# Optimization experiments

Measured on AMD Instinct MI355X. Metric: run time of the kernel, lower is better.

The kernel has to match this reference:

```python
import jax, jax.numpy as jnp
import numpy as np

BN_EPS = 1e-5


def _binary_activation(x):
    # forward value = sign(x); gradient flows through piecewise poly o3 (STE)
    s = jnp.sign(x)
    o1 = jnp.where(x < -1.0, -1.0, x * x + 2.0 * x)
    o2 = jnp.where(x < 0.0, o1, -x * x + 2.0 * x)
    o3 = jnp.where(x < 1.0, o2, 1.0)
    return jax.lax.stop_gradient(s - o3) + o3


def _binarize_weights(w):
    # sign_function: fwd 2*(w>0)-1, bwd identity (STE)
    sgn = 2.0 * (w > 0.0).astype(w.dtype) - 1.0
    wb = jax.lax.stop_gradient(sgn - w) + w
    # detached per-output-channel scale: mean |w| over (in, kh, kw)
    scale = jax.lax.stop_gradient(jnp.mean(jnp.abs(w), axis=(1, 2, 3), keepdims=True))
    return scale * wb


def setup_inputs() -> dict:
    key = jax.random.key(0)
    k1, k2, k3 = jax.random.split(key, 3)
    C = 64
    x = jax.random.normal(k1, (32, C, 112, 112), dtype=jnp.float32)
    w = jax.random.uniform(k2, (C, C, 3, 3), dtype=jnp.float32) * 0.001
    return {
        "x": x,
        "b0": jnp.zeros((1, C, 1, 1), jnp.float32),
        "w": w,
        "gamma": jnp.ones((C,), jnp.float32),
        "beta": jnp.zeros((C,), jnp.float32),
        "b1": jnp.zeros((1, C, 1, 1), jnp.float32),
        "alpha": jnp.full((C,), 0.25, jnp.float32),  # PReLU default init
        "b2": jnp.zeros((1, C, 1, 1), jnp.float32),
    }


def reference(x, b0, w, gamma, beta, b1, alpha, b2):
    residual = x
    out = x + b0                       # move0
    out = _binary_activation(out)      # binary activation
    bw = _binarize_weights(w)
    out = jax.lax.conv_general_dilated(
        out, bw, window_strides=(1, 1), padding=[(1, 1), (1, 1)],
        dimension_numbers=("NCHW", "OIHW", "NCHW"))
    # BatchNorm2d in training mode (batch stats, biased variance)
    mu = jnp.mean(out, axis=(0, 2, 3), keepdims=True)
    var = jnp.var(out, axis=(0, 2, 3), keepdims=True)
    g = gamma.reshape(1, -1, 1, 1)
    b = beta.reshape(1, -1, 1, 1)
    out = (out - mu) * jax.lax.rsqrt(var + BN_EPS) * g + b
    out = out + residual
    out = out + b1                     # move1
    a = alpha.reshape(1, -1, 1, 1)
    out = jnp.where(out > 0, out, a * out)  # PReLU
    out = out + b2                     # move2
    return out
```

## Files before the change

### kernel.cpp

```cpp
#include <hip/hip_runtime.h>
#include <stdint.h>

#define C 64
#define HH 112
#define WWD 112
#define HW (HH*WWD)
#define NB 32
#define MTOT (NB*HW)
#define PPR 56
#define PPI 6272
#define PACK_BLKS 1568
#define CONV_BLKS 25
#define OH 32
#define FL4 3136

typedef unsigned long long u64t;

__global__ __launch_bounds__(256) void k_prep_pack(
        const float* __restrict__ x, const float* __restrict__ b0,
        const float* __restrict__ w,
        uint64_t* __restrict__ xp,
        uint64_t* __restrict__ wbits, float* __restrict__ wscale,
        int* __restrict__ corrP, int* __restrict__ ps, u64t* __restrict__ pq) {
    int bid = blockIdx.x;
    if (bid < PACK_BLKS) {
        int n = bid / 49;
        int pix = (bid % 49) * 256 + threadIdx.x;
        uint64_t p = 0;
        const float* xb = x + (size_t)n * C * HW + pix;
        #pragma unroll
        for (int c = 0; c < C; ++c) {
            float v = xb[(size_t)c * HW] + b0[c];
            p |= (uint64_t)(v > 0.f) << c;
        }
        xp[(size_t)n*HW + pix] = p;
    } else {
        int tid = threadIdx.x;
        int o = bid - PACK_BLKS;
        if (tid < 64) {
            int i = tid;
            const float* wp = w + ((size_t)o*C + i)*9;
            float s = 0.f;
            uint64_t b[9];
            #pragma unroll
            for (int k = 0; k < 9; ++k) {
                float v = wp[k];
                s += fabsf(v);
                b[k] = __ballot(v > 0.f);
            }
            #pragma unroll
            for (int off = 32; off > 0; off >>= 1) s += __shfl_down(s, off);
            if (i == 0) {
                wscale[o] = s * (1.0f/576.0f);
                int pq9[9];
                #pragma unroll
                for (int k = 0; k < 9; ++k) {
                    wbits[o*9+k] = b[k];
                    pq9[k] = __popcll(b[k]);
                }
                for (int rc = 0; rc < 3; ++rc)
                    for (int cc = 0; cc < 3; ++cc) {
                        int corr = 0;
                        for (int kr = 0; kr < 3; ++kr)
                            for (int kc = 0; kc < 3; ++kc) {
                                bool oob = (rc==0 && kr==0) || (rc==2 && kr==2) ||
                                           (cc==0 && kc==0) || (cc==2 && kc==2);
                                if (oob) corr += 64 - 2*pq9[kr*3+kc];
                            }
                        corrP[(rc*3+cc)*C + o] = 576 - corr;
                    }
            }
        } else if (bid == PACK_BLKS) {
            for (int i = tid - 64; i < C*8; i += 192) { ps[i] = 0; pq[i] = 0ull; }
        }
    }
}

__global__ __launch_bounds__(256) void k_convstats(
        const uint64_t* __restrict__ xp, const uint64_t* __restrict__ wbits,
        const int* __restrict__ corrP, int* __restrict__ ps, u64t* __restrict__ pq,
        uint32_t* __restrict__ cv) {
    __shared__ uint64_t sq[OH*9];
    __shared__ int scor[9*OH];
    __shared__ int lsw[4][OH];
    __shared__ int lqw[4][OH];
    const int obase = blockIdx.z * OH;
    for (int i = threadIdx.x; i < OH*9; i += 256) sq[i] = wbits[obase*9 + i];
    for (int i = threadIdx.x; i < 9*OH; i += 256) {
        int r = i / OH, oo = i - r*OH;
        scor[i] = corrP[r*C + obase + oo];
    }
    __syncthreads();

    int n = blockIdx.y;
    int pr = blockIdx.x * 256 + threadIdx.x;
    int act = pr < PPI;
    int prc = act ? pr : (PPI - 1);
    int row = prc / PPR;
    int j   = prc - row * PPR;
    int c0  = 2 * j;
    const uint64_t* base = xp + (size_t)n * HW;
    uint64_t P[12];
    #pragma unroll
    for (int r = 0; r < 3; ++r) {
        int rr = row + r - 1;
        bool okr = (rr >= 0) & (rr < HH);
        #pragma unroll
        for (int c = 0; c < 4; ++c) {
            int cc = c0 + c - 1;
            bool ok = okr & (cc >= 0) & (cc < WWD);
            P[r*4+c] = ok ? base[(size_t)rr * WWD + cc] : 0ull;
        }
    }
    int rc   = (row == 0) ? 0 : ((row == HH-1) ? 2 : 1);
    int reg0 = (rc*3 + ((c0 == 0) ? 0 : 1)) * OH;
    int reg1 = (rc*3 + ((c0 == WWD-2) ? 2 : 1)) * OH;
    int wid = threadIdx.x >> 6, lane = threadIdx.x & 63;

    uint32_t* op = cv + ((size_t)n * C + obase) * HW + prc;

    #pragma unroll 2
    for (int oo = 0; oo < OH; ++oo) {
        const uint64_t* q = &sq[oo*9];
        int a0 = 0, a1 = 0;
        #pragma unroll
        for (int r = 0; r < 3; ++r) {
            #pragma unroll
            for (int c = 0; c < 3; ++c) {
                uint64_t qk = q[r*3+c];
                a0 += __popcll(P[r*4+c]   ^ qk);
                a1 += __popcll(P[r*4+c+1] ^ qk);
            }
        }
        int v0 = scor[reg0 + oo] - 2*a0;
        int v1 = scor[reg1 + oo] - 2*a1;
        if (act) op[(size_t)oo * HW] =
            (uint32_t)(uint16_t)v0 | ((uint32_t)(uint16_t)v1 << 16);
        int s  = act ? (v0 + v1) : 0;
        int qq = act ? (v0*v0 + v1*v1) : 0;
        #pragma unroll
        for (int off = 1; off < 64; off <<= 1) {
            s  += __shfl_xor(s,  off);
            qq += __shfl_xor(qq, off);
        }
        if (lane == 0) { lsw[wid][oo] = s; lqw[wid][oo] = qq; }
    }
    __syncthreads();
    int t = threadIdx.x;
    int bkt = blockIdx.y & 7;
    if (t < OH) {
        int st = lsw[0][t] + lsw[1][t] + lsw[2][t] + lsw[3][t];
        atomicAdd(&ps[(obase + t)*8 + bkt], st);
    } else if (t < 2*OH) {
        int oo = t - OH;
        unsigned int qt = (unsigned)lqw[0][oo] + (unsigned)lqw[1][oo]
                        + (unsigned)lqw[2][oo] + (unsigned)lqw[3][oo];
        atomicAdd(&pq[(obase + oo)*8 + bkt], (u64t)qt);
    }
}

__global__ __launch_bounds__(256) void k_finish(
        const uint32_t* __restrict__ cv, const float* __restrict__ x,
        const int* __restrict__ ps, const u64t* __restrict__ pq,
        const float* __restrict__ wscale, const float* __restrict__ gamma,
        const float* __restrict__ beta, const float* __restrict__ b1,
        const float* __restrict__ alpha, const float* __restrict__ b2,
        float* __restrict__ out) {
    int o = blockIdx.x;
    int n = blockIdx.y;
    size_t plane = (size_t)n * C + o;

    int s = 0; u64t qv = 0;
    #pragma unroll
    for (int k = 0; k < 8; ++k) { s += ps[o*8+k]; qv += pq[o*8+k]; }
    const float inv = 1.0f / (float)MTOT;
    float sc   = wscale[o];
    float mean = (float)s * inv;
    float ek2  = (float)qv * inv;
    float mu   = sc * mean;
    float var  = sc*sc*ek2 - mu*mu;
    float g    = gamma[o] * rsqrtf(var + 1e-5f);
    float A    = g * sc;
    float B    = beta[o] - g*mu + b1[o];
    float al   = alpha[o];
    float bb2  = b2[o];

    const uint2* cv2 = (const uint2*)cv + plane * (size_t)(HW/2);
    uint2 rbuf[13];
    #pragma unroll
    for (int k = 0; k < 13; ++k) {
        int i = threadIdx.x + k*256;
        if (i < FL4) rbuf[k] = cv2[i];
    }
    __syncthreads();

    const float4* x4 = (const float4*)x + plane * (size_t)FL4;
    float4*       o4 = (float4*)out     + plane * (size_t)FL4;
    #pragma unroll
    for (int k = 0; k < 13; ++k) {
        int i = threadIdx.x + k*256;
        if (i < FL4) {
            uint2 u = rbuf[k];
            float4 xv = x4[i], r;
            float t;
            t = A * (float)(int)(short)(u.x & 0xFFFF) + B + xv.x; t = t > 0.f ? t : al*t; r.x = t + bb2;
            t = A * (float)(int)(short)(u.x >> 16)    + B + xv.y; t = t > 0.f ? t : al*t; r.y = t + bb2;
            t = A * (float)(int)(short)(u.y & 0xFFFF) + B + xv.z; t = t > 0.f ? t : al*t; r.z = t + bb2;
            t = A * (float)(int)(short)(u.y >> 16)    + B + xv.w; t = t > 0.f ? t : al*t; r.w = t + bb2;
            o4[i] = r;
        }
    }
}

extern "C" void kernel_launch(void* const* d_in, const int* in_sizes, int n_in,
                              void* d_out, int out_size, void* d_ws, size_t ws_size,
                              hipStream_t stream) {
    const float* x     = (const float*)d_in[0];
    const float* b0    = (const float*)d_in[1];
    const float* w     = (const float*)d_in[2];
    const float* gamma = (const float*)d_in[3];
    const float* beta  = (const float*)d_in[4];
    const float* b1    = (const float*)d_in[5];
    const float* alpha = (const float*)d_in[6];
    const float* b2    = (const float*)d_in[7];

    char* ws = (char*)d_ws;
    const size_t XPB = (size_t)NB * HW * sizeof(uint64_t);
    uint64_t* xp     = (uint64_t*)ws;
    uint64_t* wbits  = (uint64_t*)(ws + XPB);
    u64t*     pq     = (u64t*)(ws + XPB + 4608);
    float*    wscale = (float*)(ws + XPB + 4608 + 4096);
    int*      corrP  = (int*)(ws + XPB + 4608 + 4096 + 256);
    int*      ps     = (int*)(ws + XPB + 4608 + 4096 + 256 + 2304);

    uint32_t* cv = (uint32_t*)d_out;

    hipLaunchKernelGGL(k_prep_pack, dim3(PACK_BLKS + 64), dim3(256), 0, stream,
                       x, b0, w, xp, wbits, wscale, corrP, ps, pq);
    hipLaunchKernelGGL(k_convstats, dim3(CONV_BLKS, NB, 2), dim3(256), 0, stream,
                       xp, wbits, corrP, ps, pq, cv);
    hipLaunchKernelGGL(k_finish, dim3(C, NB), dim3(256), 0, stream,
                       cv, x, ps, pq, wscale, gamma, beta, b1, alpha, b2,
                       (float*)d_out);
}
```

Before: 120.9 us.

## Replace XNOR-popcount conv with int8 MFMA conv and separate stats kernel

The binary conv no longer uses XOR/popcount on bit-packed activations. Activations are now packed as int8 signs (-1/0/+1) into holes of the output buffer, and the conv runs on mfma_i32_32x32x32_i8 with weights held in registers and input rows staged through LDS. This handles zero padding and sign(0)=0 naturally, so the border correction table goes away. Statistics move into a separate per-plane reduction kernel that replaces the atomics, which adds a launch and an extra read of the conv output. The risk is overlapping buffer aliasing in d_out between the sign rows and the conv results.

```diff
diff --git a/kernel.cpp b/kernel.cpp
--- a/kernel.cpp
+++ b/kernel.cpp
@@ -4,179 +4,184 @@
 #define C 64
 #define HH 112
 #define WWD 112
-#define HW (HH*WWD)
+#define HW 12544
 #define NB 32
 #define MTOT (NB*HW)
-#define PPR 56
-#define PPI 6272
-#define PACK_BLKS 1568
-#define CONV_BLKS 25
-#define OH 32
-#define FL4 3136
-
-typedef unsigned long long u64t;
-
-__global__ __launch_bounds__(256) void k_prep_pack(
+#define PLANE_SH 25088
+#define PLANE_BYTES 50176
+#define ROWB 7168
+#define HOLE_OFF 25088
+
+typedef int v4i  __attribute__((ext_vector_type(4)));
+typedef int v16i __attribute__((ext_vector_type(16)));
+
+__device__ __forceinline__ const char* sign_row_c(const char* outb, int R) {
+    return outb + (size_t)(R/3)*PLANE_BYTES + HOLE_OFF + (size_t)(R%3)*ROWB;
+}
+__device__ __forceinline__ char* sign_row(char* outb, int R) {
+    return outb + (size_t)(R/3)*PLANE_BYTES + HOLE_OFF + (size_t)(R%3)*ROWB;
+}
+
+__global__ __launch_bounds__(256) void k_pack(
         const float* __restrict__ x, const float* __restrict__ b0,
         const float* __restrict__ w,
-        uint64_t* __restrict__ xp,
-        uint64_t* __restrict__ wbits, float* __restrict__ wscale,
-        int* __restrict__ corrP, int* __restrict__ ps, u64t* __restrict__ pq) {
+        char* __restrict__ outb, char* __restrict__ A8, float* __restrict__ wscale) {
     int bid = blockIdx.x;
-    if (bid < PACK_BLKS) {
-        int n = bid / 49;
-        int pix = (bid % 49) * 256 + threadIdx.x;
-        uint64_t p = 0;
-        const float* xb = x + (size_t)n * C * HW + pix;
-        #pragma unroll
-        for (int c = 0; c < C; ++c) {
-            float v = xb[(size_t)c * HW] + b0[c];
-            p |= (uint64_t)(v > 0.f) << c;
-        }
-        xp[(size_t)n*HW + pix] = p;
+    if (bid < 1568) {
+        int p = bid*256 + threadIdx.x;
+        int n = p / HW, hw = p - n*HW;
+        int h = hw / WWD, wc = hw - h*WWD;
+        const float* xb = x + (size_t)n*C*HW + hw;
+        uint32_t packs[16];
+        #pragma unroll
+        for (int cq = 0; cq < 16; ++cq) {
+            uint32_t u = 0;
+            #pragma unroll
+            for (int j = 0; j < 4; ++j) {
+                int c = cq*4 + j;
+                float v = xb[(size_t)c*HW] + b0[c];
+                char sg = v > 0.f ? 1 : (v < 0.f ? -1 : 0);
+                u |= ((uint32_t)(uint8_t)sg) << (8*j);
+            }
+            packs[cq] = u;
+        }
+        uint4* d4 = (uint4*)(sign_row(outb, n*HH + h) + wc*64);
+        #pragma unroll
+        for (int j = 0; j < 4; ++j)
+            d4[j] = make_uint4(packs[j*4], packs[j*4+1], packs[j*4+2], packs[j*4+3]);
     } else {
-        int tid = threadIdx.x;
-        int o = bid - PACK_BLKS;
-        if (tid < 64) {
-            int i = tid;
-            const float* wp = w + ((size_t)o*C + i)*9;
-            float s = 0.f;
-            uint64_t b[9];
+        int t = threadIdx.x;
+        int o = t >> 2, part = t & 3;
+        float s = 0.f;
+        for (int cc = 0; cc < 16; ++cc) {
+            int c = part*16 + cc;
+            const float* wp = w + ((size_t)o*C + c)*9;
             #pragma unroll
-            for (int k = 0; k < 9; ++k) {
-                float v = wp[k];
+            for (int tap = 0; tap < 9; ++tap) {
+                float v = wp[tap];
                 s += fabsf(v);
-                b[k] = __ballot(v > 0.f);
+                A8[(o*9 + tap)*64 + c] = v > 0.f ? (char)1 : (char)-1;
             }
+        }
+        __shared__ float pabs[256];
+        pabs[t] = s;
+        __syncthreads();
+        if (t < 64)
+            wscale[t] = (pabs[t*4]+pabs[t*4+1]+pabs[t*4+2]+pabs[t*4+3]) * (1.0f/576.0f);
+    }
+}
+
+__global__ __launch_bounds__(256) void k_conv(
+        const char* __restrict__ signb, const char* __restrict__ A8,
+        short* __restrict__ cv16) {
+    __shared__ __align__(16) char lds8[4*114*80];
+    int n  = blockIdx.y;
+    int rb = blockIdx.x * 2;
+
+    for (int it = threadIdx.x; it < 4*448; it += 256) {
+        int ri = it / 448;
+        int k  = it - ri*448;
+        int col = k >> 2;
+        int b   = (k & 3) * 16;
+        int Rr = rb - 1 + ri;
+        uint4 v = make_uint4(0,0,0,0);
+        if (Rr >= 0 && Rr < HH)
+            v = ((const uint4*)sign_row_c(signb, n*HH + Rr))[k];
+        *(uint4*)&lds8[(ri*114 + col + 1)*80 + b] = v;
+    }
+    if (threadIdx.x < 32) {
+        int r   = threadIdx.x >> 3;
+        int col = ((threadIdx.x >> 2) & 1) * 113;
+        int j   = threadIdx.x & 3;
+        *(uint4*)&lds8[(r*114 + col)*80 + j*16] = make_uint4(0,0,0,0);
+    }
+
+    int lane  = threadIdx.x & 63;
+    int wv    = threadIdx.x >> 6;
+    int ot    = wv & 1;
+    int gsel  = lane >> 5;
+    int olane = ot*32 + (lane & 31);
+
+    v4i afr[9][2];
+    #pragma unroll
+    for (int tap = 0; tap < 9; ++tap) {
+        #pragma unroll
+        for (int h = 0; h < 2; ++h)
+            afr[tap][h] = *(const v4i*)(A8 + (size_t)(olane*9 + tap)*64 + h*32 + gsel*16);
+    }
+    __syncthreads();
+
+    for (int T = (wv >> 1); T < 7; T += 2) {
+        int px   = T*32 + (lane & 31);
+        int roff = px >= WWD ? 1 : 0;
+        int cpx  = px - roff*WWD;
+        v16i accA = {0,0,0,0,0,0,0,0,0,0,0,0,0,0,0,0};
+        v16i accB = {0,0,0,0,0,0,0,0,0,0,0,0,0,0,0,0};
+        #pragma unroll
+        for (int kh = 0; kh < 3; ++kh) {
             #pragma unroll
-            for (int off = 32; off > 0; off >>= 1) s += __shfl_down(s, off);
-            if (i == 0) {
-                wscale[o] = s * (1.0f/576.0f);
-                int pq9[9];
-                #pragma unroll
-                for (int k = 0; k < 9; ++k) {
-                    wbits[o*9+k] = b[k];
-                    pq9[k] = __popcll(b[k]);
-                }
-                for (int rc = 0; rc < 3; ++rc)
-                    for (int cc = 0; cc < 3; ++cc) {
-                        int corr = 0;
-                        for (int kr = 0; kr < 3; ++kr)
-                            for (int kc = 0; kc < 3; ++kc) {
-                                bool oob = (rc==0 && kr==0) || (rc==2 && kr==2) ||
-                                           (cc==0 && kc==0) || (cc==2 && kc==2);
-                                if (oob) corr += 64 - 2*pq9[kr*3+kc];
-                            }
-                        corrP[(rc*3+cc)*C + o] = 576 - corr;
-                    }
+            for (int kw = 0; kw < 3; ++kw) {
+                const char* bp = &lds8[((roff+kh)*114 + (cpx+kw))*80 + gsel*16];
+                v4i b0v = *(const v4i*)bp;
+                v4i b1v = *(const v4i*)(bp + 32);
+                accA = __builtin_amdgcn_mfma_i32_32x32x32_i8(afr[kh*3+kw][0], b0v, accA, 0, 0, 0);
+                accB = __builtin_amdgcn_mfma_i32_32x32x32_i8(afr[kh*3+kw][1], b1v, accB, 0, 0, 0);
             }
-        } else if (bid == PACK_BLKS) {
-            for (int i = tid - 64; i < C*8; i += 192) { ps[i] = 0; pq[i] = 0ull; }
-        }
-    }
-}
-
-__global__ __launch_bounds__(256) void k_convstats(
-        const uint64_t* __restrict__ xp, const uint64_t* __restrict__ wbits,
-        const int* __restrict__ corrP, int* __restrict__ ps, u64t* __restrict__ pq,
-        uint32_t* __restrict__ cv) {
-    __shared__ uint64_t sq[OH*9];
-    __shared__ int scor[9*OH];
-    __shared__ int lsw[4][OH];
-    __shared__ int lqw[4][OH];
-    const int obase = blockIdx.z * OH;
-    for (int i = threadIdx.x; i < OH*9; i += 256) sq[i] = wbits[obase*9 + i];
-    for (int i = threadIdx.x; i < 9*OH; i += 256) {
-        int r = i / OH, oo = i - r*OH;
-        scor[i] = corrP[r*C + obase + oo];
-    }
+        }
+        v16i acc = accA + accB;
+        size_t pixbase = (size_t)rb*WWD + px;
+        #pragma unroll
+        for (int r = 0; r < 16; ++r) {
+            int o = ot*32 + (r & 3) + 8*(r >> 2) + 4*gsel;
+            cv16[(size_t)(n*C + o)*PLANE_SH + pixbase] = (short)acc[r];
+        }
+    }
+}
+
+__global__ __launch_bounds__(256) void k_stats(
+        const short* __restrict__ cv16, int* __restrict__ ps,
+        long long* __restrict__ pq) {
+    int plane = blockIdx.x;
+    const uint2* p = (const uint2*)(cv16 + (size_t)plane*PLANE_SH);
+    int s = 0; unsigned q = 0;
+    for (int i = threadIdx.x; i < 3136; i += 256) {
+        uint2 u = p[i];
+        int v0 = (int)(short)(u.x & 0xFFFF), v1 = (int)(short)(u.x >> 16);
+        int v2 = (int)(short)(u.y & 0xFFFF), v3 = (int)(short)(u.y >> 16);
+        s += (v0+v1) + (v2+v3);
+        q += (unsigned)(v0*v0 + v1*v1) + (unsigned)(v2*v2 + v3*v3);
+    }
+    __shared__ int ls[256];
+    __shared__ unsigned long long lq[256];
+    ls[threadIdx.x] = s; lq[threadIdx.x] = q;
     __syncthreads();
-
-    int n = blockIdx.y;
-    int pr = blockIdx.x * 256 + threadIdx.x;
-    int act = pr < PPI;
-    int prc = act ? pr : (PPI - 1);
-    int row = prc / PPR;
-    int j   = prc - row * PPR;
-    int c0  = 2 * j;
-    const uint64_t* base = xp + (size_t)n * HW;
-    uint64_t P[12];
-    #pragma unroll
-    for (int r = 0; r < 3; ++r) {
-        int rr = row + r - 1;
-        bool okr = (rr >= 0) & (rr < HH);
-        #pragma unroll
-        for (int c = 0; c < 4; ++c) {
-            int cc = c0 + c - 1;
-            bool ok = okr & (cc >= 0) & (cc < WWD);
-            P[r*4+c] = ok ? base[(size_t)rr * WWD + cc] : 0ull;
-        }
-    }
-    int rc   = (row == 0) ? 0 : ((row == HH-1) ? 2 : 1);
-    int reg0 = (rc*3 + ((c0 == 0) ? 0 : 1)) * OH;
-    int reg1 = (rc*3 + ((c0 == WWD-2) ? 2 : 1)) * OH;
-    int wid = threadIdx.x >> 6, lane = threadIdx.x & 63;
-
-    uint32_t* op = cv + ((size_t)n * C + obase) * HW + prc;
-
-    #pragma unroll 2
-    for (int oo = 0; oo < OH; ++oo) {
-        const uint64_t* q = &sq[oo*9];
-        int a0 = 0, a1 = 0;
-        #pragma unroll
-        for (int r = 0; r < 3; ++r) {
-            #pragma unroll
-            for (int c = 0; c < 3; ++c) {
-                uint64_t qk = q[r*3+c];
-                a0 += __popcll(P[r*4+c]   ^ qk);
-                a1 += __popcll(P[r*4+c+1] ^ qk);
-            }
-        }
-        int v0 = scor[reg0 + oo] - 2*a0;
-        int v1 = scor[reg1 + oo] - 2*a1;
-        if (act) op[(size_t)oo * HW] =
-            (uint32_t)(uint16_t)v0 | ((uint32_t)(uint16_t)v1 << 16);
-        int s  = act ? (v0 + v1) : 0;
-        int qq = act ? (v0*v0 + v1*v1) : 0;
-        #pragma unroll
-        for (int off = 1; off < 64; off <<= 1) {
-            s  += __shfl_xor(s,  off);
-            qq += __shfl_xor(qq, off);
-        }
-        if (lane == 0) { lsw[wid][oo] = s; lqw[wid][oo] = qq; }
-    }
-    __syncthreads();
-    int t = threadIdx.x;
-    int bkt = blockIdx.y & 7;
-    if (t < OH) {
-        int st = lsw[0][t] + lsw[1][t] + lsw[2][t] + lsw[3][t];
-        atomicAdd(&ps[(obase + t)*8 + bkt], st);
-    } else if (t < 2*OH) {
-        int oo = t - OH;
-        unsigned int qt = (unsigned)lqw[0][oo] + (unsigned)lqw[1][oo]
-                        + (unsigned)lqw[2][oo] + (unsigned)lqw[3][oo];
-        atomicAdd(&pq[(obase + oo)*8 + bkt], (u64t)qt);
-    }
+    for (int st = 128; st > 0; st >>= 1) {
+        if ((int)threadIdx.x < st) {
+            ls[threadIdx.x] += ls[threadIdx.x+st];
+            lq[threadIdx.x] += lq[threadIdx.x+st];
+        }
+        __syncthreads();
+    }
+    if (threadIdx.x == 0) { ps[plane] = ls[0]; pq[plane] = (long long)lq[0]; }
 }
 
 __global__ __launch_bounds__(256) void k_finish(
-        const uint32_t* __restrict__ cv, const float* __restrict__ x,
-        const int* __restrict__ ps, const u64t* __restrict__ pq,
+        const short* __restrict__ cv16, const float* __restrict__ x,
+        const int* __restrict__ ps, const long long* __restrict__ pq,
         const float* __restrict__ wscale, const float* __restrict__ gamma,
         const float* __restrict__ beta, const float* __restrict__ b1,
         const float* __restrict__ alpha, const float* __restrict__ b2,
         float* __restrict__ out) {
-    int o = blockIdx.x;
-    int n = blockIdx.y;
-    size_t plane = (size_t)n * C + o;
-
-    int s = 0; u64t qv = 0;
-    #pragma unroll
-    for (int k = 0; k < 8; ++k) { s += ps[o*8+k]; qv += pq[o*8+k]; }
+    int o = blockIdx.x, n = blockIdx.y;
+    size_t plane = (size_t)n*C + o;
+
+    int s = 0; long long q = 0;
+    #pragma unroll 8
+    for (int nn = 0; nn < NB; ++nn) { s += ps[nn*C + o]; q += pq[nn*C + o]; }
     const float inv = 1.0f / (float)MTOT;
     float sc   = wscale[o];
     float mean = (float)s * inv;
-    float ek2  = (float)qv * inv;
+    float ek2  = (float)q * inv;
     float mu   = sc * mean;
     float var  = sc*sc*ek2 - mu*mu;
     float g    = gamma[o] * rsqrtf(var + 1e-5f);
@@ -185,21 +190,21 @@
     float al   = alpha[o];
     float bb2  = b2[o];
 
-    const uint2* cv2 = (const uint2*)cv + plane * (size_t)(HW/2);
+    const uint2* cv2 = (const uint2*)(cv16 + plane*PLANE_SH);
     uint2 rbuf[13];
     #pragma unroll
     for (int k = 0; k < 13; ++k) {
         int i = threadIdx.x + k*256;
-        if (i < FL4) rbuf[k] = cv2[i];
+        if (i < 3136) rbuf[k] = cv2[i];
     }
     __syncthreads();
 
-    const float4* x4 = (const float4*)x + plane * (size_t)FL4;
-    float4*       o4 = (float4*)out     + plane * (size_t)FL4;
+    const float4* x4 = (const float4*)x + plane*3136;
+    float4*       o4 = (float4*)out     + plane*3136;
     #pragma unroll
     for (int k = 0; k < 13; ++k) {
         int i = threadIdx.x + k*256;
-        if (i < FL4) {
+        if (i < 3136) {
             uint2 u = rbuf[k];
             float4 xv = x4[i], r;
             float t;
@@ -225,21 +230,21 @@
     const float* b2    = (const float*)d_in[7];
 
     char* ws = (char*)d_ws;
-    const size_t XPB = (size_t)NB * HW * sizeof(uint64_t);
-    uint64_t* xp     = (uint64_t*)ws;
-    uint64_t* wbits  = (uint64_t*)(ws + XPB);
-    u64t*     pq     = (u64t*)(ws + XPB + 4608);
-    float*    wscale = (float*)(ws + XPB + 4608 + 4096);
-    int*      corrP  = (int*)(ws + XPB + 4608 + 4096 + 256);
-    int*      ps     = (int*)(ws + XPB + 4608 + 4096 + 256 + 2304);
-
-    uint32_t* cv = (uint32_t*)d_out;
-
-    hipLaunchKernelGGL(k_prep_pack, dim3(PACK_BLKS + 64), dim3(256), 0, stream,
-                       x, b0, w, xp, wbits, wscale, corrP, ps, pq);
-    hipLaunchKernelGGL(k_convstats, dim3(CONV_BLKS, NB, 2), dim3(256), 0, stream,
-                       xp, wbits, corrP, ps, pq, cv);
-    hipLaunchKernelGGL(k_finish, dim3(C, NB), dim3(256), 0, stream,
-                       cv, x, ps, pq, wscale, gamma, beta, b1, alpha, b2,
+    char*      A8     = ws;
+    float*     wscale = (float*)(ws + 36864);
+    int*       ps     = (int*)(ws + 37120);
+    long long* pq     = (long long*)(ws + 45312);
+
+    char*  outb = (char*)d_out;
+    short* cv16 = (short*)d_out;
+
+    hipLaunchKernelGGL(k_pack, dim3(1569), dim3(256), 0, stream,
+                       x, b0, w, outb, A8, wscale);
+    hipLaunchKernelGGL(k_conv, dim3(56, 32), dim3(256), 0, stream,
+                       outb, A8, cv16);
+    hipLaunchKernelGGL(k_stats, dim3(2048), dim3(256), 0, stream,
+                       cv16, ps, pq);
+    hipLaunchKernelGGL(k_finish, dim3(64, 32), dim3(256), 0, stream,
+                       cv16, x, ps, pq, wscale, gamma, beta, b1, alpha, b2,
                        (float*)d_out);
 }
```

Result: no change. 122.0 us (+0.9%).
